# Optimization experiments

Hardware: AMD Instinct MI355X
Metric: run time of the kernel (lower is better)

The kernel has to match this reference:

```python
import jax, jax.numpy as jnp
import numpy as np

V, D, C, B, S, H = 50000, 256, 10, 64, 512, 512


def setup_inputs() -> dict:
    key = jax.random.key(0)
    ks = jax.random.split(key, 12)
    s = 0.02
    return {
        "x": jax.random.randint(ks[0], (B, S), 0, V),
        "embed_w": jax.random.normal(ks[1], (V, D), dtype=jnp.float32) * s,
        "Wl": jax.random.normal(ks[2], (D, D), dtype=jnp.float32) * s,
        "bl": jnp.zeros((D,), jnp.float32),
        "Wsl": jax.random.normal(ks[3], (D, D), dtype=jnp.float32) * s,
        "bsl": jnp.zeros((D,), jnp.float32),
        "Wr": jax.random.normal(ks[4], (D, D), dtype=jnp.float32) * s,
        "br": jnp.zeros((D,), jnp.float32),
        "Wsr": jax.random.normal(ks[5], (D, D), dtype=jnp.float32) * s,
        "bsr": jnp.zeros((D,), jnp.float32),
        "conv_w": jax.random.normal(ks[6], (H, 3 * D), dtype=jnp.float32) * s,
        "conv_b": jnp.zeros((H,), jnp.float32),
        "fc_w": jax.random.normal(ks[7], (C, H), dtype=jnp.float32) * s,
        "fc_b": jnp.zeros((C,), jnp.float32),
        "cl0": jax.random.normal(ks[8], (B, D), dtype=jnp.float32),
        "cr0": jax.random.normal(ks[9], (B, D), dtype=jnp.float32),
    }


def reference(x, embed_w, Wl, bl, Wsl, bsl, Wr, br, Wsr, bsr,
              conv_w, conv_b, fc_w, fc_b, cl0, cr0):
    e = embed_w[x]  # [B,S,D] embedding lookup
    # Precompute the embedding-dependent half of each recurrence (one big GEMM)
    pre_l = jnp.swapaxes(jnp.einsum("bsd,ed->bse", e, Wsl) + bsl, 0, 1)  # [S,B,D]
    pre_r = jnp.swapaxes(jnp.einsum("bsd,ed->bse", e, Wsr) + bsr, 0, 1)  # [S,B,D]

    # left[0]=cl0; left[t]=relu(Wl left[t-1] + Wsl e[t-1])  (output carry, then update)
    def lstep(c, p):
        return jax.nn.relu(c @ Wl.T + bl + p), c

    _, left = jax.lax.scan(lstep, cl0, pre_l)  # [S,B,D]

    # right[S-1]=cr0; right[t]=relu(Wr right[t+1] + Wsr e[t+1])
    def rstep(c, p):
        return jax.nn.relu(c @ Wr.T + br + p), c

    _, right = jax.lax.scan(rstep, cr0, pre_r, reverse=True)  # [S,B,D]

    ctx = jnp.concatenate(
        [jnp.swapaxes(left, 0, 1), e, jnp.swapaxes(right, 0, 1)], axis=-1
    )  # [B,S,3D]
    # Conv2d(1,512,(1,3D)) == per-timestep linear 3D->512
    h = jax.nn.relu(jnp.einsum("bsd,hd->bsh", ctx, conv_w) + conv_b)  # [B,S,H]
    pooled = h.max(axis=1)  # max_pool1d over full sequence -> [B,H]
    return pooled @ fc_w.T + fc_b  # [B,C]
```

## Files before the change

### kernel.cpp

```cpp
#include <hip/hip_runtime.h>
#include <hip/hip_bf16.h>

#define VOCAB 50000
#define DD 256
#define NCLS 10
#define BB 64
#define SS 512
#define HH 512
#define K3D 768

typedef __attribute__((ext_vector_type(8))) short bf16x8;
typedef __attribute__((ext_vector_type(8))) unsigned short ush8;
typedef __attribute__((ext_vector_type(4))) float f32x4;

static __device__ __forceinline__ unsigned short f2bf(float f) {
    __hip_bfloat16 h = __float2bfloat16(f);
    return *reinterpret_cast<unsigned short*>(&h);
}

static __device__ __forceinline__ ush8 cvt8(const float* src) {
    const float4 lo = *(const float4*)(src);
    const float4 hi = *(const float4*)(src + 4);
    uint4 u;
    asm("v_cvt_pk_bf16_f32 %0, %1, %2" : "=v"(u.x) : "v"(lo.x), "v"(lo.y));
    asm("v_cvt_pk_bf16_f32 %0, %1, %2" : "=v"(u.y) : "v"(lo.z), "v"(lo.w));
    asm("v_cvt_pk_bf16_f32 %0, %1, %2" : "=v"(u.z) : "v"(hi.x), "v"(hi.y));
    asm("v_cvt_pk_bf16_f32 %0, %1, %2" : "=v"(u.w) : "v"(hi.z), "v"(hi.w));
    return *reinterpret_cast<ush8*>(&u);
}

#define PPAD 72

__global__ __launch_bounds__(256) void prep_pre_kernel(
    const float* __restrict__ Wsl, const float* __restrict__ Wsr,
    const float* __restrict__ bsl, const float* __restrict__ bl,
    const float* __restrict__ bsr, const float* __restrict__ br,
    const int* __restrict__ x, const float* __restrict__ embed_w,
    const float* __restrict__ conv_w,
    unsigned short* __restrict__ convwb,
    float* __restrict__ pre2_l, float* __restrict__ pre2_r,
    float* __restrict__ pooled)
{
    __shared__ unsigned short Abuf[2][128][PPAD];
    __shared__ unsigned short Bbuf[2][128][PPAD];
    __shared__ int xs[128];

    const int bid = blockIdx.x;
    const int tid = threadIdx.x;

    if (bid < 1024) {
        const int mi  = bid >> 8;
        const int sbi = bid & 255;
        const int w = tid >> 6, lane = tid & 63;
        const int lr = lane & 15, g = lane >> 4;
        const int lk = g * 8;
        const int strow = tid >> 3;
        const int skc   = (tid & 7) * 8;

        if (tid < 128)
            xs[tid] = x[(tid & 63) * SS + 2 * sbi + (tid >> 6)];

        f32x4 acc[2][8];
#pragma unroll
        for (int mt = 0; mt < 2; ++mt)
#pragma unroll
            for (int nt = 0; nt < 8; ++nt) acc[mt][nt] = (f32x4)(0.f);

        auto stage = [&](int ks, int buf) {
            const int k0 = ks * 64;
#pragma unroll
            for (int j = 0; j < 4; ++j) {
                const int row = strow + 32 * j;
                const float* wsrc = (mi < 2 ? Wsl + (size_t)(mi * 128 + row) * DD
                                            : Wsr + (size_t)((mi - 2) * 128 + row) * DD)
                                    + k0 + skc;
                *(ush8*)&Abuf[buf][row][skc] = cvt8(wsrc);
                const float* esrc = embed_w + (size_t)xs[row] * DD + k0 + skc;
                *(ush8*)&Bbuf[buf][row][skc] = cvt8(esrc);
            }
        };

        __syncthreads();
        stage(0, 0);
        int cur = 0;
        for (int ks = 0; ks < 4; ++ks) {
            __syncthreads();
            if (ks + 1 < 4) stage(ks + 1, cur ^ 1);
#pragma unroll
            for (int k2 = 0; k2 < 2; ++k2) {
                const int kk = k2 * 32 + lk;
                const bf16x8 a0 = *(const bf16x8*)&Abuf[cur][w * 32 + lr][kk];
                const bf16x8 a1 = *(const bf16x8*)&Abuf[cur][w * 32 + 16 + lr][kk];
#pragma unroll
                for (int nt = 0; nt < 8; ++nt) {
                    const bf16x8 bv = *(const bf16x8*)&Bbuf[cur][nt * 16 + lr][kk];
                    acc[0][nt] = __builtin_amdgcn_mfma_f32_16x16x32_bf16(a0, bv, acc[0][nt], 0, 0, 0);
                    acc[1][nt] = __builtin_amdgcn_mfma_f32_16x16x32_bf16(a1, bv, acc[1][nt], 0, 0, 0);
                }
            }
            cur ^= 1;
        }

#pragma unroll
        for (int mt = 0; mt < 2; ++mt) {
            const int eg = mi * 128 + w * 32 + mt * 16 + g * 4;
            const int e  = eg & 255;
            const float* bsx = (eg < 256) ? bsl : bsr;
            const float* bbx = (eg < 256) ? bl  : br;
            const float4 b1 = *(const float4*)(bsx + e);
            const float4 b2 = *(const float4*)(bbx + e);
            float* dstb = (eg >= 256) ? pre2_r : pre2_l;
#pragma unroll
            for (int nt = 0; nt < 8; ++nt) {
                const int sb = sbi * 128 + nt * 16 + lr;
                const int s = sb >> 6, bgq = (sb >> 4) & 3, b_loc = sb & 15;
                float4 v;
                v.x = acc[mt][nt][0] + b1.x + b2.x;
                v.y = acc[mt][nt][1] + b1.y + b2.y;
                v.z = acc[mt][nt][2] + b1.z + b2.z;
                v.w = acc[mt][nt][3] + b1.w + b2.w;
                *(float4*)(dstb + ((size_t)s * 4 + bgq) * 4096 + (e >> 2) * 64 + b_loc * 4) = v;
            }
        }
    } else if (bid < 1216) {
        const int g = (bid - 1024) * 256 + tid;
        *(ush8*)(convwb + (size_t)g * 8) = cvt8(conv_w + (size_t)g * 8);
    } else {
        float4* p = (float4*)pooled;
#pragma unroll
        for (int i = 0; i < 32; ++i)
            p[tid + 256 * i] = make_float4(0.f, 0.f, 0.f, 0.f);
    }
}

#define CSWZ(row, off) ((off) ^ (((row) & 15) << 4))
#define APAD 72

__global__ __launch_bounds__(256, 1) void recur_conve_kernel(
    const float* __restrict__ Wl, const float* __restrict__ Wr,
    const float* __restrict__ cl0, const float* __restrict__ cr0,
    const float* __restrict__ pre2_l, const float* __restrict__ pre2_r,
    unsigned short* __restrict__ outl, unsigned short* __restrict__ outr,
    const int* __restrict__ x, const float* __restrict__ embed_w,
    const unsigned short* __restrict__ convwb,
    unsigned short* __restrict__ hpart)
{
    __shared__ alignas(16) unsigned char smem[2 * 2 * 128 * APAD * 2];
    __shared__ int xsv[512];

    const int tid  = threadIdx.x;
    const int lane = tid & 63;

    if (blockIdx.x < 8) {
        unsigned short* cbf0 = (unsigned short*)smem;
        unsigned short* cbf1 = (unsigned short*)smem + 16 * 256;

        const int dir = blockIdx.x >> 2;
        const int bg  = blockIdx.x & 3;
        const int b0  = bg * 16;
        const int wl  = tid >> 6;
        const int col = lane & 15;
        const int g   = lane >> 4;

        const float* W   = dir ? Wr : Wl;
        const float* c0  = dir ? cr0 : cl0;
        const float* pre = dir ? pre2_r : pre2_l;
        unsigned short* out = dir ? outr : outl;

        bf16x8 wfrag[4][8];
#pragma unroll
        for (int mt = 0; mt < 4; ++mt)
#pragma unroll
            for (int i = 0; i < 8; ++i) {
                const int kt = (i + 2 * wl) & 7;
                const float* src = W + (size_t)(wl * 64 + mt * 16 + col) * DD
                                     + kt * 32 + g * 8;
                const ush8 p = cvt8(src);
                wfrag[mt][i] = *(bf16x8*)&p;
            }

        int soff[8];
#pragma unroll
        for (int i = 0; i < 8; ++i) {
            const int kt = (i + 2 * wl) & 7;
            soff[i] = CSWZ(col, kt * 64 + g * 16);
        }

        {
            const int blc = tid >> 4;
            const int ch  = tid & 15;
            const float* src = c0 + (size_t)(b0 + blc) * DD + ch * 16;
            const ush8 p0 = cvt8(src);
            const ush8 p1 = cvt8(src + 8);
            char* rowp = (char*)cbf0 + blc * 512;
            *(ush8*)(rowp + CSWZ(blc, ch * 32))      = p0;
            *(ush8*)(rowp + CSWZ(blc, ch * 32 + 16)) = p1;
            const int t0 = dir ? 511 : 0;
            ush8* dst = (ush8*)(out + ((size_t)t0 * BB + b0 + blc) * DD + ch * 16);
            dst[0] = p0; dst[1] = p1;
        }

        const int lpre = (wl * 16 + g) * 64 + col * 4;
        const ptrdiff_t pstep = dir ? -(ptrdiff_t)16384 : (ptrdiff_t)16384;
        const float* p0 = pre + ((size_t)(dir ? 511 : 0) * 4 + bg) * 4096 + lpre;

        float4 pA0 = *(const float4*)(p0);
        float4 pA1 = *(const float4*)(p0 + 256);
        float4 pA2 = *(const float4*)(p0 + 512);
        float4 pA3 = *(const float4*)(p0 + 768);
        const float* p1p = p0 + pstep;
        float4 pB0 = *(const float4*)(p1p);
        float4 pB1 = *(const float4*)(p1p + 256);
        float4 pB2 = *(const float4*)(p1p + 512);
        float4 pB3 = *(const float4*)(p1p + 768);
        const float* pfetch = p0 + 2 * pstep;

        unsigned short* oplane = out + (size_t)(dir ? 510 : 1) * BB * DD
                                     + (b0 + col) * DD + wl * 64 + g * 4;
        const ptrdiff_t ostep = (dir ? -(ptrdiff_t)1 : (ptrdiff_t)1) * (BB * DD);

        __syncthreads();

        int cur = 0;
#pragma unroll 2
        for (int k = 0; k < SS - 1; ++k) {
            bf16x8 sfrag[8];
            {
                const char* rowp = (const char*)(cur ? cbf1 : cbf0) + col * 512;
#pragma unroll
                for (int i = 0; i < 8; ++i)
                    sfrag[i] = *(const bf16x8*)(rowp + soff[i]);
            }

            const float4 pN0 = *(const float4*)(pfetch);
            const float4 pN1 = *(const float4*)(pfetch + 256);
            const float4 pN2 = *(const float4*)(pfetch + 512);
            const float4 pN3 = *(const float4*)(pfetch + 768);
            if (k < SS - 4) pfetch += pstep;

            char* nbuf = (char*)(cur ? cbf0 : cbf1) + col * 512;

            auto epi = [&](int mt, const f32x4 a) {
                const float v0 = fmaxf(a[0], 0.f);
                const float v1 = fmaxf(a[1], 0.f);
                const float v2 = fmaxf(a[2], 0.f);
                const float v3 = fmaxf(a[3], 0.f);
                uint2 uu;
                asm("v_cvt_pk_bf16_f32 %0, %1, %2" : "=v"(uu.x) : "v"(v0), "v"(v1));
                asm("v_cvt_pk_bf16_f32 %0, %1, %2" : "=v"(uu.y) : "v"(v2), "v"(v3));
                const int eoff = (wl * 64 + mt * 16 + g * 4) * 2;
                *(uint2*)(nbuf + CSWZ(col, eoff)) = uu;
                *(uint2*)(oplane + mt * 16) = uu;
            };

            f32x4 a0 = *(const f32x4*)&pA0;
            f32x4 a1 = *(const f32x4*)&pA1;
            __builtin_amdgcn_s_setprio(1);
#pragma unroll
            for (int i = 0; i < 8; ++i) {
                a0 = __builtin_amdgcn_mfma_f32_16x16x32_bf16(wfrag[0][i], sfrag[i], a0, 0, 0, 0);
                a1 = __builtin_amdgcn_mfma_f32_16x16x32_bf16(wfrag[1][i], sfrag[i], a1, 0, 0, 0);
            }
            __builtin_amdgcn_s_setprio(0);
            epi(0, a0);
            epi(1, a1);

            f32x4 a2 = *(const f32x4*)&pA2;
            f32x4 a3 = *(const f32x4*)&pA3;
            __builtin_amdgcn_s_setprio(1);
#pragma unroll
            for (int i = 0; i < 8; ++i) {
                a2 = __builtin_amdgcn_mfma_f32_16x16x32_bf16(wfrag[2][i], sfrag[i], a2, 0, 0, 0);
                a3 = __builtin_amdgcn_mfma_f32_16x16x32_bf16(wfrag[3][i], sfrag[i], a3, 0, 0, 0);
            }
            __builtin_amdgcn_s_setprio(0);
            epi(2, a2);
            epi(3, a3);

            pA0 = pB0; pA1 = pB1; pA2 = pB2; pA3 = pB3;
            pB0 = pN0; pB1 = pN1; pB2 = pN2; pB3 = pN3;
            oplane += ostep;

            asm volatile("s_waitcnt lgkmcnt(0)" ::: "memory");
            __builtin_amdgcn_s_barrier();
            asm volatile("" ::: "memory");
            cur ^= 1;
        }
        return;
    }

    unsigned short* Ab = (unsigned short*)smem;
    unsigned short* Bb = (unsigned short*)smem + 2 * 128 * APAD;

    const int wid = tid >> 6;
    const int lr  = lane & 15;
    const int lk  = (lane >> 4) * 8;
    const int strow = tid >> 3;
    const int skc   = (tid & 7) * 8;

    for (int rep = 0; rep < 2; ++rep) {
        const int cid = (blockIdx.x - 8) + rep * 128;
        const int b   = cid >> 2;
        const int h0  = (cid & 3) * 128;

        for (int i = tid; i < SS; i += 256) xsv[i] = x[b * SS + i];
        __syncthreads();

        f32x4 acc[2][8];
#pragma unroll
        for (int st = 0; st < 2; ++st)
#pragma unroll
            for (int ht = 0; ht < 8; ++ht) acc[st][ht] = (f32x4)(0.f);

        auto stage = [&](int it, int buf) {
            const int stile = it >> 2, kstep = it & 3;
            const int k0 = kstep * 64;
            const int s0 = stile * 128;
#pragma unroll
            for (int j = 0; j < 4; ++j) {
                const int row = strow + 32 * j;
                const int ss = s0 + row;
                const float* esrc = embed_w + (size_t)xsv[ss] * DD + k0 + skc;
                *(ush8*)&Ab[(buf * 128 + row) * APAD + skc] = cvt8(esrc);
                *(bf16x8*)&Bb[(buf * 128 + row) * APAD + skc] =
                    *(const bf16x8*)(convwb + (size_t)(h0 + row) * K3D + 256 + k0 + skc);
            }
        };

        stage(0, 0);
        int cur = 0;
        for (int it = 0; it < 16; ++it) {
            __syncthreads();
            if (it + 1 < 16) stage(it + 1, cur ^ 1);

            const int wrow0 = wid * 32;
#pragma unroll
            for (int ks = 0; ks < 2; ++ks) {
                const int kk = ks * 32 + lk;
                const bf16x8 a0 = *(const bf16x8*)&Ab[(cur * 128 + wrow0 + lr) * APAD + kk];
                const bf16x8 a1 = *(const bf16x8*)&Ab[(cur * 128 + wrow0 + 16 + lr) * APAD + kk];
#pragma unroll
                for (int ht = 0; ht < 8; ++ht) {
                    const bf16x8 bv = *(const bf16x8*)&Bb[(cur * 128 + ht * 16 + lr) * APAD + kk];
                    acc[0][ht] = __builtin_amdgcn_mfma_f32_16x16x32_bf16(a0, bv, acc[0][ht], 0, 0, 0);
                    acc[1][ht] = __builtin_amdgcn_mfma_f32_16x16x32_bf16(a1, bv, acc[1][ht], 0, 0, 0);
                }
            }
            if ((it & 3) == 3) {
                const int stile = it >> 2;
                unsigned short* hp = hpart + (size_t)(cid * 4 + stile) * 16384;
#pragma unroll
                for (int st = 0; st < 2; ++st)
#pragma unroll
                    for (int ht = 0; ht < 8; ++ht) {
                        uint2 uu;
                        asm("v_cvt_pk_bf16_f32 %0, %1, %2"
                            : "=v"(uu.x) : "v"(acc[st][ht][0]), "v"(acc[st][ht][1]));
                        asm("v_cvt_pk_bf16_f32 %0, %1, %2"
                            : "=v"(uu.y) : "v"(acc[st][ht][2]), "v"(acc[st][ht][3]));
                        const int f = (wid * 2 + st) * 8 + ht;
                        *(uint2*)(hp + f * 256 + lane * 4) = uu;
                        acc[st][ht] = (f32x4)(0.f);
                    }
            }
            cur ^= 1;
        }
        __syncthreads();
    }
}

#define KSTEP 64
#define NKC 8

__global__ __launch_bounds__(256) void conv_pool_kernel(
    const unsigned short* __restrict__ leftb,
    const unsigned short* __restrict__ rightb,
    const unsigned short* __restrict__ convwb,
    const unsigned short* __restrict__ hpart,
    const float* __restrict__ conv_b,
    float* __restrict__ pooled)
{
    __shared__ unsigned short Abuf[2][128][APAD];
    __shared__ unsigned short Bbuf[2][128][APAD];
    __shared__ float red[4][128];

    const int stile = blockIdx.x & 3;
    const int h0i   = (blockIdx.x >> 2) & 3;
    const int b     = blockIdx.x >> 4;
    const int h0    = h0i * 128;
    const int s0    = stile * 128;
    const int tid = threadIdx.x;
    const int wid = tid >> 6;
    const int lane = tid & 63;
    const int lr  = lane & 15;
    const int lk  = (lane >> 4) * 8;
    const int strow = tid >> 3;
    const int skc   = (tid & 7) * 8;

    f32x4 acc[2][8];
    {
        const unsigned short* hp = hpart
            + ((size_t)((b * 4 + h0i) * 4 + stile)) * 16384;
#pragma unroll
        for (int st = 0; st < 2; ++st)
#pragma unroll
            for (int ht = 0; ht < 8; ++ht) {
                const int f = (wid * 2 + st) * 8 + ht;
                const uint2 uu = *(const uint2*)(hp + f * 256 + lane * 4);
                f32x4 v;
                v[0] = __uint_as_float(uu.x << 16);
                v[1] = __uint_as_float(uu.x & 0xffff0000u);
                v[2] = __uint_as_float(uu.y << 16);
                v[3] = __uint_as_float(uu.y & 0xffff0000u);
                acc[st][ht] = v;
            }
    }

    auto stage = [&](int kstep, int buf) {
        const int k0 = kstep * KSTEP;
        const unsigned short* asrc;
        int koff, bcol;
        if (k0 < DD) { asrc = leftb;  koff = k0;      bcol = k0; }
        else         { asrc = rightb; koff = k0 - DD; bcol = k0 + 256; }
#pragma unroll
        for (int j = 0; j < 4; ++j) {
            const int row = strow + 32 * j;
            const int ss = s0 + row;
            *(bf16x8*)&Abuf[buf][row][skc] =
                *(const bf16x8*)(asrc + ((size_t)ss * BB + b) * DD + koff + skc);
            *(bf16x8*)&Bbuf[buf][row][skc] =
                *(const bf16x8*)(convwb + (size_t)(h0 + row) * K3D + bcol + skc);
        }
    };

    stage(0, 0);
    int cur = 0;
    for (int it = 0; it < NKC; ++it) {
        __syncthreads();
        if (it + 1 < NKC) stage(it + 1, cur ^ 1);

        const int wrow0 = wid * 32;
#pragma unroll
        for (int ks = 0; ks < 2; ++ks) {
            const int kk = ks * 32 + lk;
            const bf16x8 a0 = *(const bf16x8*)&Abuf[cur][wrow0 + lr][kk];
            const bf16x8 a1 = *(const bf16x8*)&Abuf[cur][wrow0 + 16 + lr][kk];
#pragma unroll
            for (int ht = 0; ht < 8; ++ht) {
                const bf16x8 bv = *(const bf16x8*)&Bbuf[cur][ht * 16 + lr][kk];
                acc[0][ht] = __builtin_amdgcn_mfma_f32_16x16x32_bf16(a0, bv, acc[0][ht], 0, 0, 0);
                acc[1][ht] = __builtin_amdgcn_mfma_f32_16x16x32_bf16(a1, bv, acc[1][ht], 0, 0, 0);
            }
        }
        cur ^= 1;
    }

    float pmax[8];
#pragma unroll
    for (int ht = 0; ht < 8; ++ht) {
        float m = -INFINITY;
#pragma unroll
        for (int st = 0; st < 2; ++st)
#pragma unroll
            for (int r = 0; r < 4; ++r)
                m = fmaxf(m, acc[st][ht][r]);
        m = fmaxf(m, __shfl_xor(m, 16));
        m = fmaxf(m, __shfl_xor(m, 32));
        if (lane < 16) red[wid][ht * 16 + lane] = m;
    }
    __syncthreads();
    if (tid < 128) {
        const float m = fmaxf(fmaxf(red[0][tid], red[1][tid]),
                              fmaxf(red[2][tid], red[3][tid]));
        const float v = fmaxf(m + conv_b[h0 + tid], 0.f);
        atomicMax((unsigned*)(pooled + (size_t)b * HH + h0 + tid),
                  __float_as_uint(v));
    }
}

__global__ void fc_kernel(const float* __restrict__ pooled,
                          const float* __restrict__ fc_w,
                          const float* __restrict__ fc_b,
                          float* __restrict__ out)
{
    const int t = threadIdx.x;
    if (t >= BB * NCLS) return;
    const int b = t / NCLS, c = t % NCLS;
    float acc = fc_b[c];
    for (int h = 0; h < HH; ++h)
        acc += pooled[(size_t)b * HH + h] * fc_w[(size_t)c * HH + h];
    out[b * NCLS + c] = acc;
}

extern "C" void kernel_launch(void* const* d_in, const int* in_sizes, int n_in,
                              void* d_out, int out_size, void* d_ws, size_t ws_size,
                              hipStream_t stream)
{
    const int*   x       = (const int*)  d_in[0];
    const float* embed_w = (const float*)d_in[1];
    const float* Wl      = (const float*)d_in[2];
    const float* bl      = (const float*)d_in[3];
    const float* Wsl     = (const float*)d_in[4];
    const float* bsl     = (const float*)d_in[5];
    const float* Wr      = (const float*)d_in[6];
    const float* br      = (const float*)d_in[7];
    const float* Wsr     = (const float*)d_in[8];
    const float* bsr     = (const float*)d_in[9];
    const float* conv_w  = (const float*)d_in[10];
    const float* conv_b  = (const float*)d_in[11];
    const float* fc_w    = (const float*)d_in[12];
    const float* fc_b    = (const float*)d_in[13];
    const float* cl0     = (const float*)d_in[14];
    const float* cr0     = (const float*)d_in[15];
    float* out = (float*)d_out;

    char* ws = (char*)d_ws;
    const size_t SZf = (size_t)SS * BB * DD * sizeof(float);
    const size_t SZh = (size_t)SS * BB * DD * sizeof(unsigned short);
    float*          pre2_l = (float*)(ws);
    float*          pre2_r = (float*)(ws + SZf);
    unsigned short* leftb  = (unsigned short*)(ws + 2 * SZf);
    unsigned short* rightb = (unsigned short*)(ws + 2 * SZf + SZh);
    unsigned short* convwb = (unsigned short*)(ws + 2 * SZf + 2 * SZh);
    float*          pooled = (float*)(ws + 2 * SZf + 2 * SZh + (size_t)HH * K3D * 2);
    unsigned short* hpart  = (unsigned short*)(ws + 2 * SZf + 2 * SZh
                                               + (size_t)HH * K3D * 2
                                               + (size_t)BB * HH * 4);

    prep_pre_kernel<<<1217, 256, 0, stream>>>(
        Wsl, Wsr, bsl, bl, bsr, br, x, embed_w, conv_w,
        convwb, pre2_l, pre2_r, pooled);

    recur_conve_kernel<<<136, 256, 0, stream>>>(
        Wl, Wr, cl0, cr0, pre2_l, pre2_r, leftb, rightb,
        x, embed_w, convwb, hpart);

    conv_pool_kernel<<<1024, 256, 0, stream>>>(
        leftb, rightb, convwb, hpart, conv_b, pooled);

    fc_kernel<<<1, BB * NCLS, 0, stream>>>(pooled, fc_w, fc_b, out);
}
```

Measured before the change: 421.6 us.

## Store precomputed recurrence inputs as bf16 and parallelize fc across blocks

The precomputed embedding projections (pre2_l/pre2_r) are now written as packed bf16 instead of fp32. This halves the bytes the prep kernel writes and the latency-bound recurrence loop reads each step, at the cost of lower precision in the recurrence input. The fc kernel is also rewritten from a single block of serial dot products into 64 blocks, each doing warp-split partial sums with a shuffle reduction.

```diff
diff --git a/kernel.cpp b/kernel.cpp
--- a/kernel.cpp
+++ b/kernel.cpp
@@ -29,6 +29,15 @@
     return *reinterpret_cast<ush8*>(&u);
 }
 
+static __device__ __forceinline__ f32x4 unpk(uint2 u) {
+    f32x4 v;
+    v[0] = __uint_as_float(u.x << 16);
+    v[1] = __uint_as_float(u.x & 0xffff0000u);
+    v[2] = __uint_as_float(u.y << 16);
+    v[3] = __uint_as_float(u.y & 0xffff0000u);
+    return v;
+}
+
 #define PPAD 72
 
 __global__ __launch_bounds__(256) void prep_pre_kernel(
@@ -38,7 +47,7 @@
     const int* __restrict__ x, const float* __restrict__ embed_w,
     const float* __restrict__ conv_w,
     unsigned short* __restrict__ convwb,
-    float* __restrict__ pre2_l, float* __restrict__ pre2_r,
+    unsigned short* __restrict__ pre2_l, unsigned short* __restrict__ pre2_r,
     float* __restrict__ pooled)
 {
     __shared__ unsigned short Abuf[2][128][PPAD];
@@ -109,17 +118,19 @@
             const float* bbx = (eg < 256) ? bl  : br;
             const float4 b1 = *(const float4*)(bsx + e);
             const float4 b2 = *(const float4*)(bbx + e);
-            float* dstb = (eg >= 256) ? pre2_r : pre2_l;
+            unsigned short* dstb = (eg >= 256) ? pre2_r : pre2_l;
 #pragma unroll
             for (int nt = 0; nt < 8; ++nt) {
                 const int sb = sbi * 128 + nt * 16 + lr;
                 const int s = sb >> 6, bgq = (sb >> 4) & 3, b_loc = sb & 15;
-                float4 v;
-                v.x = acc[mt][nt][0] + b1.x + b2.x;
-                v.y = acc[mt][nt][1] + b1.y + b2.y;
-                v.z = acc[mt][nt][2] + b1.z + b2.z;
-                v.w = acc[mt][nt][3] + b1.w + b2.w;
-                *(float4*)(dstb + ((size_t)s * 4 + bgq) * 4096 + (e >> 2) * 64 + b_loc * 4) = v;
+                const float vx = acc[mt][nt][0] + b1.x + b2.x;
+                const float vy = acc[mt][nt][1] + b1.y + b2.y;
+                const float vz = acc[mt][nt][2] + b1.z + b2.z;
+                const float vw = acc[mt][nt][3] + b1.w + b2.w;
+                uint2 uu;
+                asm("v_cvt_pk_bf16_f32 %0, %1, %2" : "=v"(uu.x) : "v"(vx), "v"(vy));
+                asm("v_cvt_pk_bf16_f32 %0, %1, %2" : "=v"(uu.y) : "v"(vz), "v"(vw));
+                *(uint2*)(dstb + ((size_t)s * 4 + bgq) * 4096 + (e >> 2) * 64 + b_loc * 4) = uu;
             }
         }
     } else if (bid < 1216) {
@@ -139,7 +150,8 @@
 __global__ __launch_bounds__(256, 1) void recur_conve_kernel(
     const float* __restrict__ Wl, const float* __restrict__ Wr,
     const float* __restrict__ cl0, const float* __restrict__ cr0,
-    const float* __restrict__ pre2_l, const float* __restrict__ pre2_r,
+    const unsigned short* __restrict__ pre2_l,
+    const unsigned short* __restrict__ pre2_r,
     unsigned short* __restrict__ outl, unsigned short* __restrict__ outr,
     const int* __restrict__ x, const float* __restrict__ embed_w,
     const unsigned short* __restrict__ convwb,
@@ -164,7 +176,7 @@
 
         const float* W   = dir ? Wr : Wl;
         const float* c0  = dir ? cr0 : cl0;
-        const float* pre = dir ? pre2_r : pre2_l;
+        const unsigned short* pre = dir ? pre2_r : pre2_l;
         unsigned short* out = dir ? outr : outl;
 
         bf16x8 wfrag[4][8];
@@ -202,18 +214,19 @@
 
         const int lpre = (wl * 16 + g) * 64 + col * 4;
         const ptrdiff_t pstep = dir ? -(ptrdiff_t)16384 : (ptrdiff_t)16384;
-        const float* p0 = pre + ((size_t)(dir ? 511 : 0) * 4 + bg) * 4096 + lpre;
-
-        float4 pA0 = *(const float4*)(p0);
-        float4 pA1 = *(const float4*)(p0 + 256);
-        float4 pA2 = *(const float4*)(p0 + 512);
-        float4 pA3 = *(const float4*)(p0 + 768);
-        const float* p1p = p0 + pstep;
-        float4 pB0 = *(const float4*)(p1p);
-        float4 pB1 = *(const float4*)(p1p + 256);
-        float4 pB2 = *(const float4*)(p1p + 512);
-        float4 pB3 = *(const float4*)(p1p + 768);
-        const float* pfetch = p0 + 2 * pstep;
+        const unsigned short* p0 = pre
+            + ((size_t)(dir ? 511 : 0) * 4 + bg) * 4096 + lpre;
+
+        uint2 pA0 = *(const uint2*)(p0);
+        uint2 pA1 = *(const uint2*)(p0 + 256);
+        uint2 pA2 = *(const uint2*)(p0 + 512);
+        uint2 pA3 = *(const uint2*)(p0 + 768);
+        const unsigned short* p1p = p0 + pstep;
+        uint2 pB0 = *(const uint2*)(p1p);
+        uint2 pB1 = *(const uint2*)(p1p + 256);
+        uint2 pB2 = *(const uint2*)(p1p + 512);
+        uint2 pB3 = *(const uint2*)(p1p + 768);
+        const unsigned short* pfetch = p0 + 2 * pstep;
 
         unsigned short* oplane = out + (size_t)(dir ? 510 : 1) * BB * DD
                                      + (b0 + col) * DD + wl * 64 + g * 4;
@@ -232,10 +245,10 @@
                     sfrag[i] = *(const bf16x8*)(rowp + soff[i]);
             }
 
-            const float4 pN0 = *(const float4*)(pfetch);
-            const float4 pN1 = *(const float4*)(pfetch + 256);
-            const float4 pN2 = *(const float4*)(pfetch + 512);
-            const float4 pN3 = *(const float4*)(pfetch + 768);
+            const uint2 pN0 = *(const uint2*)(pfetch);
+            const uint2 pN1 = *(const uint2*)(pfetch + 256);
+            const uint2 pN2 = *(const uint2*)(pfetch + 512);
+            const uint2 pN3 = *(const uint2*)(pfetch + 768);
             if (k < SS - 4) pfetch += pstep;
 
             char* nbuf = (char*)(cur ? cbf0 : cbf1) + col * 512;
@@ -253,8 +266,8 @@
                 *(uint2*)(oplane + mt * 16) = uu;
             };
 
-            f32x4 a0 = *(const f32x4*)&pA0;
-            f32x4 a1 = *(const f32x4*)&pA1;
+            f32x4 a0 = unpk(pA0);
+            f32x4 a1 = unpk(pA1);
             __builtin_amdgcn_s_setprio(1);
 #pragma unroll
             for (int i = 0; i < 8; ++i) {
@@ -265,8 +278,8 @@
             epi(0, a0);
             epi(1, a1);
 
-            f32x4 a2 = *(const f32x4*)&pA2;
-            f32x4 a3 = *(const f32x4*)&pA3;
+            f32x4 a2 = unpk(pA2);
+            f32x4 a3 = unpk(pA3);
             __builtin_amdgcn_s_setprio(1);
 #pragma unroll
             for (int i = 0; i < 8; ++i) {
@@ -407,12 +420,7 @@
             for (int ht = 0; ht < 8; ++ht) {
                 const int f = (wid * 2 + st) * 8 + ht;
                 const uint2 uu = *(const uint2*)(hp + f * 256 + lane * 4);
-                f32x4 v;
-                v[0] = __uint_as_float(uu.x << 16);
-                v[1] = __uint_as_float(uu.x & 0xffff0000u);
-                v[2] = __uint_as_float(uu.y << 16);
-                v[3] = __uint_as_float(uu.y & 0xffff0000u);
-                acc[st][ht] = v;
+                acc[st][ht] = unpk(uu);
             }
     }
 
@@ -478,18 +486,29 @@
     }
 }
 
-__global__ void fc_kernel(const float* __restrict__ pooled,
-                          const float* __restrict__ fc_w,
-                          const float* __restrict__ fc_b,
-                          float* __restrict__ out)
+__global__ __launch_bounds__(320) void fc_kernel(
+    const float* __restrict__ pooled,
+    const float* __restrict__ fc_w,
+    const float* __restrict__ fc_b,
+    float* __restrict__ out)
 {
-    const int t = threadIdx.x;
-    if (t >= BB * NCLS) return;
-    const int b = t / NCLS, c = t % NCLS;
-    float acc = fc_b[c];
-    for (int h = 0; h < HH; ++h)
-        acc += pooled[(size_t)b * HH + h] * fc_w[(size_t)c * HH + h];
-    out[b * NCLS + c] = acc;
+    const int b = blockIdx.x;
+    const int c = threadIdx.x >> 5;
+    const int l = threadIdx.x & 31;
+    const float* pb = pooled + (size_t)b * HH;
+    const float* wc = fc_w + (size_t)c * HH;
+    float acc = 0.f;
+#pragma unroll
+    for (int i = 0; i < 16; ++i) {
+        const int h = l + 32 * i;
+        acc += pb[h] * wc[h];
+    }
+    acc += __shfl_xor(acc, 1);
+    acc += __shfl_xor(acc, 2);
+    acc += __shfl_xor(acc, 4);
+    acc += __shfl_xor(acc, 8);
+    acc += __shfl_xor(acc, 16);
+    if (l == 0) out[b * NCLS + c] = acc + fc_b[c];
 }
 
 extern "C" void kernel_launch(void* const* d_in, const int* in_sizes, int n_in,
@@ -515,15 +534,14 @@
     float* out = (float*)d_out;
 
     char* ws = (char*)d_ws;
-    const size_t SZf = (size_t)SS * BB * DD * sizeof(float);
     const size_t SZh = (size_t)SS * BB * DD * sizeof(unsigned short);
-    float*          pre2_l = (float*)(ws);
-    float*          pre2_r = (float*)(ws + SZf);
-    unsigned short* leftb  = (unsigned short*)(ws + 2 * SZf);
-    unsigned short* rightb = (unsigned short*)(ws + 2 * SZf + SZh);
-    unsigned short* convwb = (unsigned short*)(ws + 2 * SZf + 2 * SZh);
-    float*          pooled = (float*)(ws + 2 * SZf + 2 * SZh + (size_t)HH * K3D * 2);
-    unsigned short* hpart  = (unsigned short*)(ws + 2 * SZf + 2 * SZh
+    unsigned short* pre2_l = (unsigned short*)(ws);
+    unsigned short* pre2_r = (unsigned short*)(ws + SZh);
+    unsigned short* leftb  = (unsigned short*)(ws + 2 * SZh);
+    unsigned short* rightb = (unsigned short*)(ws + 3 * SZh);
+    unsigned short* convwb = (unsigned short*)(ws + 4 * SZh);
+    float*          pooled = (float*)(ws + 4 * SZh + (size_t)HH * K3D * 2);
+    unsigned short* hpart  = (unsigned short*)(ws + 4 * SZh
                                                + (size_t)HH * K3D * 2
                                                + (size_t)BB * HH * 4);
 
@@ -538,5 +556,5 @@
     conv_pool_kernel<<<1024, 256, 0, stream>>>(
         leftb, rightb, convwb, hpart, conv_b, pooled);
 
-    fc_kernel<<<1, BB * NCLS, 0, stream>>>(pooled, fc_w, fc_b, out);
-}
+    fc_kernel<<<BB, 320, 0, stream>>>(pooled, fc_w, fc_b, out);
+}
```

New measurement: 369.5 us. 1.14x faster.
